# Performance work log

Hardware: AMD Instinct MI355X
Metric: run time of the kernel (lower is better)

The kernel has to match this reference:

```python
import jax, jax.numpy as jnp
import numpy as np

N, E = 20000, 160000
D_NODE_IN, D_EDGE_IN = 256, 64
D = 128          # node/edge feature dim
H = 256          # edge hidden dim
T = 17           # number of keypoint types
EDGE_STEPS, NODE_STEPS = 2, 1


def _w(k, shape):
    return jax.random.normal(k, shape, dtype=jnp.float32) / np.sqrt(shape[-2] if len(shape) > 1 else shape[-1]).astype(np.float32)


def setup_inputs() -> dict:
    key = jax.random.key(0)
    ks = iter(jax.random.split(key, 40))
    inp = {
        'x': jax.random.normal(next(ks), (N, D_NODE_IN), dtype=jnp.float32),
        'edge_attr': jax.random.normal(next(ks), (E, D_EDGE_IN), dtype=jnp.float32),
        'edge_index': jax.random.randint(next(ks), (2, E), 0, N),
        'node_types': jax.random.randint(next(ks), (N,), 0, T),
        # type-routed node embedding: 17 stacked 2-layer MLPs 256->128->128
        'ne_w1': _w(next(ks), (T, D_NODE_IN, D)), 'ne_b1': jnp.zeros((T, D)),
        'ne_w2': _w(next(ks), (T, D, D)),         'ne_b2': jnp.zeros((T, D)),
        # edge embedding 64->128->128
        'ee_w1': _w(next(ks), (D_EDGE_IN, D)), 'ee_b1': jnp.zeros((D,)),
        'ee_w2': _w(next(ks), (D, D)),         'ee_b2': jnp.zeros((D,)),
        # MPLayer edge MLP: [x_i, x_j, e] with skip -> (2*2D + 2D)=768 -> 256 -> 128
        'me_w1': _w(next(ks), (4 * D + 2 * D, H)), 'me_b1': jnp.zeros((H,)),
        'me_w2': _w(next(ks), (H, D)),             'me_b2': jnp.zeros((D,)),
        # MPLayer node update: [x(skip 2D), agg(D)] -> 128
        'mn_w1': _w(next(ks), (2 * D + D, D)), 'mn_b1': jnp.zeros((D,)),
        # classifiers
        'ec_w1': _w(next(ks), (D, D)), 'ec_b1': jnp.zeros((D,)),
        'ec_w2': _w(next(ks), (D, 1)), 'ec_b2': jnp.zeros((1,)),
        'nc_w1': _w(next(ks), (D, D)), 'nc_b1': jnp.zeros((D,)),
        'nc_w2': _w(next(ks), (D, 1)), 'nc_b2': jnp.zeros((1,)),
        'cc_w1': _w(next(ks), (D, D)), 'cc_b1': jnp.zeros((D,)),
        'cc_w2': _w(next(ks), (D, T)), 'cc_b2': jnp.zeros((T,)),
    }
    return inp


def _mlp2(x, w1, b1, w2, b2):
    return jax.nn.relu(x @ w1 + b1) @ w2 + b2


def reference(x, edge_attr, edge_index, node_types,
              ne_w1, ne_b1, ne_w2, ne_b2,
              ee_w1, ee_b1, ee_w2, ee_b2,
              me_w1, me_b1, me_w2, me_b2,
              mn_w1, mn_b1,
              ec_w1, ec_b1, ec_w2, ec_b2,
              nc_w1, nc_b1, nc_w2, nc_b2,
              cc_w1, cc_b1, cc_w2, cc_b2):
    n = x.shape[0]
    # NodeMlpType: run all 17 MLPs, select by node type (same math as masked dispatch)
    h = jax.nn.relu(jnp.einsum('nd,tdk->tnk', x, ne_w1) + ne_b1[:, None, :])   # [T,N,D]
    o = jnp.einsum('tnk,tkm->tnm', h, ne_w2) + ne_b2[:, None, :]               # [T,N,D]
    nf0 = o[node_types, jnp.arange(n)]                                          # [N,D]
    ef0 = _mlp2(edge_attr, ee_w1, ee_b1, ee_w2, ee_b2)                          # [E,D]

    src, dst = edge_index[0], edge_index[1]

    def mp_step(nf, ef):
        nf_c = jnp.concatenate([nf0, nf], axis=1)                               # skip concat [N,2D]
        ef_c = jnp.concatenate([ef0, ef], axis=1)                               # [E,2D]
        m = jnp.concatenate([nf_c[dst], nf_c[src], ef_c], axis=1)               # [E,6D]
        e_new = _mlp2(m, me_w1, me_b1, me_w2, me_b2)                            # [E,D]
        agg = jax.ops.segment_sum(e_new, dst, num_segments=n)                   # aggr='add'
        nf_new = jnp.concatenate([nf_c, agg], axis=1) @ mn_w1 + mn_b1           # [N,D]
        return nf_new, e_new

    nf, ef = nf0, ef0
    for _ in range(EDGE_STEPS):
        nf, ef = mp_step(nf, ef)
    pred_edge = _mlp2(ef, ec_w1, ec_b1, ec_w2, ec_b2).squeeze(-1)               # [E]
    for _ in range(NODE_STEPS):
        nf, ef = mp_step(nf, ef)
    pred_node = _mlp2(nf, nc_w1, nc_b1, nc_w2, nc_b2).squeeze(-1)               # [N]
    pred_class = _mlp2(nf, cc_w1, cc_b1, cc_w2, cc_b2)                          # [N,T]
    return (pred_edge, pred_node, pred_class, nf, ef)
```

## Files before the change

### kernel.cpp

```cpp
#include <hip/hip_runtime.h>
#include <hip/hip_bf16.h>

#define N_NODES 20000
#define N_EDGES 160000
#define DIN_NODE 256
#define DIN_EDGE 64
#define DF 128
#define HH 256
#define TT 17
#define NE_PAD_SLOTS 20544

typedef __attribute__((ext_vector_type(8))) short short8v;
typedef __attribute__((ext_vector_type(4))) float f32x4;

__device__ __forceinline__ unsigned short f2bf(float f) {
  unsigned int u = __builtin_bit_cast(unsigned int, f);
  u += 0x7FFFu + ((u >> 16) & 1u);
  return (unsigned short)(u >> 16);
}

__device__ __forceinline__ float bf2f(unsigned short u) {
  return __builtin_bit_cast(float, (unsigned int)u << 16);
}

__device__ __forceinline__ short8v pack8(float4 a, float4 b) {
  short8v o;
  o[0] = (short)f2bf(a.x); o[1] = (short)f2bf(a.y);
  o[2] = (short)f2bf(a.z); o[3] = (short)f2bf(a.w);
  o[4] = (short)f2bf(b.x); o[5] = (short)f2bf(b.y);
  o[6] = (short)f2bf(b.z); o[7] = (short)f2bf(b.w);
  return o;
}

__global__ __launch_bounds__(256) void k_pack_w(
    const float* __restrict__ w, unsigned short* __restrict__ out,
    int Kdim, int Ndim, int batch) {
  const int tile = blockIdx.x * 4 + (threadIdx.x >> 6);
  const int l = threadIdx.x & 63;
  const int ntTiles = Ndim >> 4;
  const int tilesPer = (Kdim >> 5) * ntTiles;
  if (tile >= tilesPer * batch) return;
  const int bt = tile / tilesPer;
  const int rr = tile - bt * tilesPer;
  const int kt = rr / ntTiles, nt = rr % ntTiles;
  const float* wb = w + (size_t)bt * Kdim * Ndim;
  const int col = (nt << 4) + (l & 15);
  const int k0 = (kt << 5) + ((l >> 4) << 3);
  unsigned short* o = out + (((size_t)tile << 6) + l) * 8;
#pragma unroll
  for (int j = 0; j < 8; ++j) o[j] = f2bf(wb[(size_t)(k0 + j) * Ndim + col]);
}

__global__ void k_count(const int* __restrict__ types, int* __restrict__ cnt) {
  const int n = blockIdx.x * 256 + threadIdx.x;
  if (n < N_NODES) atomicAdd(&cnt[types[n]], 1);
}
__global__ void k_prefix(const int* __restrict__ cnt, int* __restrict__ poff,
                         int* __restrict__ woff) {
  if (threadIdx.x == 0) {
    int cur = 0;
    for (int t = 0; t < TT; ++t) {
      poff[t] = cur; woff[t] = cur;
      cur += (cnt[t] + 31) & ~31;
    }
  }
}
__global__ void k_scatter(const int* __restrict__ types, int* __restrict__ woff,
                          int* __restrict__ bucket) {
  const int n = blockIdx.x * 256 + threadIdx.x;
  if (n < N_NODES) {
    const int pos = atomicAdd(&woff[types[n]], 1);
    bucket[pos] = n;
  }
}

__global__ void k_deg(const int* __restrict__ dstv, int* __restrict__ deg) {
  const int e = blockIdx.x * 256 + threadIdx.x;
  if (e < N_EDGES) atomicAdd(&deg[dstv[e]], 1);
}
__global__ __launch_bounds__(256) void k_scan(const int* __restrict__ deg,
                                              int* __restrict__ rs,
                                              int* __restrict__ wo) {
  __shared__ int partial[256];
  const int t = threadIdx.x;
  const int base = t * 80;
  int s = 0;
  for (int j = 0; j < 80; ++j) {
    const int n = base + j;
    if (n < N_NODES) s += deg[n];
  }
  partial[t] = s;
  __syncthreads();
  for (int off = 1; off < 256; off <<= 1) {
    const int v = (t >= off) ? partial[t - off] : 0;
    __syncthreads();
    partial[t] += v;
    __syncthreads();
  }
  int run = (t > 0) ? partial[t - 1] : 0;
  for (int j = 0; j < 80; ++j) {
    const int n = base + j;
    if (n < N_NODES) {
      rs[n] = run; wo[n] = run;
      run += deg[n];
    }
  }
  if (t == 255) rs[N_NODES] = run;
}
__global__ void k_elist(const int* __restrict__ dstv, int* __restrict__ wo,
                        int* __restrict__ elist, int* __restrict__ ipos) {
  const int e = blockIdx.x * 256 + threadIdx.x;
  if (e < N_EDGES) {
    const int pos = atomicAdd(&wo[dstv[e]], 1);
    elist[pos] = e;
    ipos[e] = pos;
  }
}
__global__ void k_perm_sd(const int* __restrict__ elist,
                          const int* __restrict__ srcv,
                          const int* __restrict__ dstv,
                          int* __restrict__ srcp, int* __restrict__ dstp) {
  const int p = blockIdx.x * 256 + threadIdx.x;
  if (p < N_EDGES) {
    const int e = elist[p];
    srcp[p] = srcv[e];
    dstp[p] = dstv[e];
  }
}

__global__ __launch_bounds__(256) void k_node_embed_mfma(
    const float* __restrict__ x, const int* __restrict__ bucket,
    const int* __restrict__ types,
    const unsigned short* __restrict__ wp1, const float* __restrict__ b1,
    const unsigned short* __restrict__ wp2, const float* __restrict__ b2,
    unsigned short* __restrict__ nf0b) {
  __shared__ __align__(16) unsigned char A[32 * 512];
  __shared__ __align__(16) unsigned char Hb[32 * 256];
  __shared__ int sn[32];
  const int t = threadIdx.x;
  const int r0 = blockIdx.x * 32;
  if (t < 32) sn[t] = bucket[r0 + t];
  __syncthreads();
  if (sn[0] < 0) return;
  const int ty = types[sn[0]];

#pragma unroll
  for (int j = 0; j < 4; ++j) {
    const int q = j * 256 + t;
    const int i = q >> 5, c = q & 31;
    const int nd = sn[i];
    short8v o;
    if (nd >= 0) {
      const float* xr = x + (size_t)nd * DIN_NODE + c * 8;
      o = pack8(*reinterpret_cast<const float4*>(xr),
                *reinterpret_cast<const float4*>(xr + 4));
    } else {
#pragma unroll
      for (int k = 0; k < 8; ++k) o[k] = 0;
    }
    *reinterpret_cast<short8v*>(A + ((i * 512 + c * 16) ^ ((i & 7) << 4))) = o;
  }
  __syncthreads();

  const int w = t >> 6, l = t & 63, lr = l & 15, lg = l >> 4;
  const int sw = (lr & 7) << 4;
  const int row0 = lr, row1 = 16 + lr;

  f32x4 acc[2][2];
#pragma unroll
  for (int mt = 0; mt < 2; ++mt)
#pragma unroll
    for (int q = 0; q < 2; ++q)
#pragma unroll
      for (int r = 0; r < 4; ++r) acc[mt][q][r] = 0.f;

#pragma unroll
  for (int kt = 0; kt < 8; ++kt) {
    const short8v a0 = *reinterpret_cast<const short8v*>(
        A + ((row0 * 512 + kt * 64 + lg * 16) ^ sw));
    const short8v a1 = *reinterpret_cast<const short8v*>(
        A + ((row1 * 512 + kt * 64 + lg * 16) ^ sw));
#pragma unroll
    for (int q = 0; q < 2; ++q) {
      const short8v bq = *reinterpret_cast<const short8v*>(
          wp1 + (((size_t)(ty * 64 + kt * 8 + 2 * w + q) * 64 + l) << 3));
      acc[0][q] = __builtin_amdgcn_mfma_f32_16x16x32_bf16(a0, bq, acc[0][q], 0, 0, 0);
      acc[1][q] = __builtin_amdgcn_mfma_f32_16x16x32_bf16(a1, bq, acc[1][q], 0, 0, 0);
    }
  }
#pragma unroll
  for (int q = 0; q < 2; ++q) {
    const int col = (2 * w + q) * 16 + lr;
    const float bias = b1[ty * DF + col];
#pragma unroll
    for (int mt = 0; mt < 2; ++mt)
#pragma unroll
      for (int r = 0; r < 4; ++r) {
        const int row = mt * 16 + lg * 4 + r;
        *reinterpret_cast<unsigned short*>(
            Hb + ((row * 256 + col * 2) ^ ((row & 7) << 4))) =
            f2bf(fmaxf(acc[mt][q][r] + bias, 0.f));
      }
  }
  __syncthreads();

  f32x4 acc2[2][2];
#pragma unroll
  for (int mt = 0; mt < 2; ++mt)
#pragma unroll
    for (int q = 0; q < 2; ++q)
#pragma unroll
      for (int r = 0; r < 4; ++r) acc2[mt][q][r] = 0.f;
#pragma unroll
  for (int kt = 0; kt < 4; ++kt) {
    const short8v a0 = *reinterpret_cast<const short8v*>(
        Hb + ((row0 * 256 + kt * 64 + lg * 16) ^ sw));
    const short8v a1 = *reinterpret_cast<const short8v*>(
        Hb + ((row1 * 256 + kt * 64 + lg * 16) ^ sw));
#pragma unroll
    for (int q = 0; q < 2; ++q) {
      const short8v bq = *reinterpret_cast<const short8v*>(
          wp2 + (((size_t)(ty * 32 + kt * 8 + 2 * w + q) * 64 + l) << 3));
      acc2[0][q] = __builtin_amdgcn_mfma_f32_16x16x32_bf16(a0, bq, acc2[0][q], 0, 0, 0);
      acc2[1][q] = __builtin_amdgcn_mfma_f32_16x16x32_bf16(a1, bq, acc2[1][q], 0, 0, 0);
    }
  }
#pragma unroll
  for (int q = 0; q < 2; ++q) {
    const int col = (2 * w + q) * 16 + lr;
    const float bias = b2[ty * DF + col];
#pragma unroll
    for (int mt = 0; mt < 2; ++mt)
#pragma unroll
      for (int r = 0; r < 4; ++r) {
        const int row = mt * 16 + lg * 4 + r;
        const int nd = sn[row];
        if (nd >= 0)
          nf0b[(size_t)nd * DF + col] = f2bf(acc2[mt][q][r] + bias);
      }
  }
}

__global__ __launch_bounds__(256) void k_edge_embed_mfma(
    const float* __restrict__ ea, const int* __restrict__ ipos,
    const unsigned short* __restrict__ wp1, const float* __restrict__ b1,
    const unsigned short* __restrict__ wp2, const float* __restrict__ b2,
    unsigned short* __restrict__ ef0p) {
  __shared__ __align__(16) unsigned char A[32 * 128];
  __shared__ __align__(16) unsigned char Hb[32 * 256];
  __shared__ int ip[32];
  const int t = threadIdx.x;
  const int e0 = blockIdx.x * 32;
  if (t < 32) ip[t] = ipos[e0 + t];
  {
    const int i = t >> 3, c = t & 7;
    const float* xr = ea + (size_t)(e0 + i) * DIN_EDGE + c * 8;
    const short8v o = pack8(*reinterpret_cast<const float4*>(xr),
                            *reinterpret_cast<const float4*>(xr + 4));
    *reinterpret_cast<short8v*>(A + ((i * 128 + c * 16) ^ ((i & 7) << 4))) = o;
  }
  __syncthreads();

  const int w = t >> 6, l = t & 63, lr = l & 15, lg = l >> 4;
  const int sw = (lr & 7) << 4;
  const int row0 = lr, row1 = 16 + lr;

  f32x4 acc[2][2];
#pragma unroll
  for (int mt = 0; mt < 2; ++mt)
#pragma unroll
    for (int q = 0; q < 2; ++q)
#pragma unroll
      for (int r = 0; r < 4; ++r) acc[mt][q][r] = 0.f;
#pragma unroll
  for (int kt = 0; kt < 2; ++kt) {
    const short8v a0 = *reinterpret_cast<const short8v*>(
        A + ((row0 * 128 + kt * 64 + lg * 16) ^ sw));
    const short8v a1 = *reinterpret_cast<const short8v*>(
        A + ((row1 * 128 + kt * 64 + lg * 16) ^ sw));
#pragma unroll
    for (int q = 0; q < 2; ++q) {
      const short8v bq = *reinterpret_cast<const short8v*>(
          wp1 + (((size_t)(kt * 8 + 2 * w + q) * 64 + l) << 3));
      acc[0][q] = __builtin_amdgcn_mfma_f32_16x16x32_bf16(a0, bq, acc[0][q], 0, 0, 0);
      acc[1][q] = __builtin_amdgcn_mfma_f32_16x16x32_bf16(a1, bq, acc[1][q], 0, 0, 0);
    }
  }
#pragma unroll
  for (int q = 0; q < 2; ++q) {
    const int col = (2 * w + q) * 16 + lr;
    const float bias = b1[col];
#pragma unroll
    for (int mt = 0; mt < 2; ++mt)
#pragma unroll
      for (int r = 0; r < 4; ++r) {
        const int row = mt * 16 + lg * 4 + r;
        *reinterpret_cast<unsigned short*>(
            Hb + ((row * 256 + col * 2) ^ ((row & 7) << 4))) =
            f2bf(fmaxf(acc[mt][q][r] + bias, 0.f));
      }
  }
  __syncthreads();

  f32x4 acc2[2][2];
#pragma unroll
  for (int mt = 0; mt < 2; ++mt)
#pragma unroll
    for (int q = 0; q < 2; ++q)
#pragma unroll
      for (int r = 0; r < 4; ++r) acc2[mt][q][r] = 0.f;
#pragma unroll
  for (int kt = 0; kt < 4; ++kt) {
    const short8v a0 = *reinterpret_cast<const short8v*>(
        Hb + ((row0 * 256 + kt * 64 + lg * 16) ^ sw));
    const short8v a1 = *reinterpret_cast<const short8v*>(
        Hb + ((row1 * 256 + kt * 64 + lg * 16) ^ sw));
#pragma unroll
    for (int q = 0; q < 2; ++q) {
      const short8v bq = *reinterpret_cast<const short8v*>(
          wp2 + (((size_t)(kt * 8 + 2 * w + q) * 64 + l) << 3));
      acc2[0][q] = __builtin_amdgcn_mfma_f32_16x16x32_bf16(a0, bq, acc2[0][q], 0, 0, 0);
      acc2[1][q] = __builtin_amdgcn_mfma_f32_16x16x32_bf16(a1, bq, acc2[1][q], 0, 0, 0);
    }
  }
#pragma unroll
  for (int q = 0; q < 2; ++q) {
    const int col = (2 * w + q) * 16 + lr;
    const float bias = b2[col];
#pragma unroll
    for (int mt = 0; mt < 2; ++mt)
#pragma unroll
      for (int r = 0; r < 4; ++r) {
        const int row = mt * 16 + lg * 4 + r;
        ef0p[(size_t)ip[row] * DF + col] = f2bf(acc2[mt][q][r] + bias);
      }
  }
}

__global__ __launch_bounds__(256) void k_partial(
    const unsigned short* __restrict__ nf0b, const unsigned short* __restrict__ nfb,
    const unsigned short* __restrict__ wpd, const unsigned short* __restrict__ wps,
    unsigned short* __restrict__ PDo, unsigned short* __restrict__ PSo) {
  __shared__ __align__(16) unsigned char A[32 * 512];
  const int t = threadIdx.x;
  const int n0 = blockIdx.x * 32;
#pragma unroll
  for (int j = 0; j < 4; ++j) {
    const int q = j * 256 + t;
    const int i = q >> 5, c = q & 31;
    const unsigned short* bp = (c < 16)
        ? nf0b + (size_t)(n0 + i) * DF + c * 8
        : nfb + (size_t)(n0 + i) * DF + (c - 16) * 8;
    *reinterpret_cast<short8v*>(A + ((i * 512 + c * 16) ^ ((i & 7) << 4))) =
        *reinterpret_cast<const short8v*>(bp);
  }
  __syncthreads();

  const int w = t >> 6, l = t & 63, lr = l & 15, lg = l >> 4;
  const int swz = (lr & 7) << 4;
  const int r0o = lr * 512 + lg * 16, r1o = (16 + lr) * 512 + lg * 16;

  f32x4 aD[2][4], aS[2][4];
#pragma unroll
  for (int mt = 0; mt < 2; ++mt)
#pragma unroll
    for (int q = 0; q < 4; ++q)
#pragma unroll
      for (int r = 0; r < 4; ++r) { aD[mt][q][r] = 0.f; aS[mt][q][r] = 0.f; }

#pragma unroll
  for (int kt = 0; kt < 8; ++kt) {
    const short8v a0 = *reinterpret_cast<const short8v*>(A + ((r0o + kt * 64) ^ swz));
    const short8v a1 = *reinterpret_cast<const short8v*>(A + ((r1o + kt * 64) ^ swz));
#pragma unroll
    for (int q = 0; q < 4; ++q) {
      const size_t bi = (((size_t)(kt * 16 + 4 * w + q) * 64 + l) << 3);
      const short8v bD = *reinterpret_cast<const short8v*>(wpd + bi);
      const short8v bS = *reinterpret_cast<const short8v*>(wps + bi);
      aD[0][q] = __builtin_amdgcn_mfma_f32_16x16x32_bf16(a0, bD, aD[0][q], 0, 0, 0);
      aD[1][q] = __builtin_amdgcn_mfma_f32_16x16x32_bf16(a1, bD, aD[1][q], 0, 0, 0);
      aS[0][q] = __builtin_amdgcn_mfma_f32_16x16x32_bf16(a0, bS, aS[0][q], 0, 0, 0);
      aS[1][q] = __builtin_amdgcn_mfma_f32_16x16x32_bf16(a1, bS, aS[1][q], 0, 0, 0);
    }
  }
#pragma unroll
  for (int q = 0; q < 4; ++q) {
    const int col = (4 * w + q) * 16 + lr;
#pragma unroll
    for (int mt = 0; mt < 2; ++mt)
#pragma unroll
      for (int r = 0; r < 4; ++r) {
        const int row = mt * 16 + lg * 4 + r;
        PDo[(size_t)(n0 + row) * HH + col] = f2bf(aD[mt][q][r]);
        PSo[(size_t)(n0 + row) * HH + col] = f2bf(aS[mt][q][r]);
      }
  }
}

template <bool OUTF, bool HEAD>
__global__ __launch_bounds__(256) void k_edge_mlp_mfma(
    const unsigned short* __restrict__ ef0, const unsigned short* __restrict__ ef_in,
    unsigned short* __restrict__ ef_out, float* __restrict__ ef_outf,
    const int* __restrict__ srcp, const int* __restrict__ dstp,
    const int* __restrict__ elist,
    const unsigned short* __restrict__ wpe, const float* __restrict__ b1,
    const unsigned short* __restrict__ wp2, const float* __restrict__ b2,
    const unsigned short* __restrict__ PDi, const unsigned short* __restrict__ PSi,
    const unsigned short* __restrict__ wech, const float* __restrict__ hb1,
    const float* __restrict__ hw2, const float* __restrict__ hb2,
    float* __restrict__ out_pe) {
  __shared__ __align__(16) unsigned char A_lds[32 * 512];
  __shared__ __align__(16) unsigned char P_lds[32 * 512];
  __shared__ int sd[2][32];
  __shared__ int se[32];
  __shared__ float hpart[32][8];
  const int t = threadIdx.x;
  const int e0 = blockIdx.x * 32;
  if (t < 32) sd[0][t] = srcp[e0 + t];
  else if (t < 64) sd[1][t - 32] = dstp[e0 + t - 32];
  else if ((OUTF || HEAD) && t < 96) se[t - 64] = elist[e0 + t - 64];

#pragma unroll
  for (int j = 0; j < 4; ++j) {
    const int q = j * 256 + t;
    const int i = q >> 5, c = q & 31;
    const unsigned short* bp = (c < 16)
        ? ef0 + (size_t)(e0 + i) * DF + c * 8
        : ef_in + (size_t)(e0 + i) * DF + (c - 16) * 8;
    *reinterpret_cast<short8v*>(A_lds + ((i * 512 + c * 16) ^ ((i & 7) << 4))) =
        *reinterpret_cast<const short8v*>(bp);
  }
  __syncthreads();

#pragma unroll
  for (int j = 0; j < 4; ++j) {
    const int q = j * 256 + t;
    const int i = q >> 5, c = q & 31;
    const short8v pd = *reinterpret_cast<const short8v*>(
        PDi + (size_t)sd[1][i] * HH + c * 8);
    const short8v ps = *reinterpret_cast<const short8v*>(
        PSi + (size_t)sd[0][i] * HH + c * 8);
    short8v o;
#pragma unroll
    for (int k = 0; k < 8; ++k)
      o[k] = (short)f2bf(bf2f((unsigned short)pd[k]) + bf2f((unsigned short)ps[k]));
    *reinterpret_cast<short8v*>(P_lds + ((i * 512 + c * 16) ^ ((i & 7) << 4))) = o;
  }
  __syncthreads();
// ... 501 lines not shown
  const float* x         = (const float*)d_in[0];
  const float* edge_attr = (const float*)d_in[1];
  const int*   edge_idx  = (const int*)d_in[2];
  const int*   node_ty   = (const int*)d_in[3];
  const float* ne_w1 = (const float*)d_in[4];
  const float* ne_b1 = (const float*)d_in[5];
  const float* ne_w2 = (const float*)d_in[6];
  const float* ne_b2 = (const float*)d_in[7];
  const float* ee_w1 = (const float*)d_in[8];
  const float* ee_b1 = (const float*)d_in[9];
  const float* ee_w2 = (const float*)d_in[10];
  const float* ee_b2 = (const float*)d_in[11];
  const float* me_w1 = (const float*)d_in[12];
  const float* me_b1 = (const float*)d_in[13];
  const float* me_w2 = (const float*)d_in[14];
  const float* me_b2 = (const float*)d_in[15];
  const float* mn_w1 = (const float*)d_in[16];
  const float* mn_b1 = (const float*)d_in[17];
  const float* ec_w1 = (const float*)d_in[18];
  const float* ec_b1 = (const float*)d_in[19];
  const float* ec_w2 = (const float*)d_in[20];
  const float* ec_b2 = (const float*)d_in[21];
  const float* nc_w1 = (const float*)d_in[22];
  const float* nc_b1 = (const float*)d_in[23];
  const float* nc_w2 = (const float*)d_in[24];
  const float* nc_b2 = (const float*)d_in[25];
  const float* cc_w1 = (const float*)d_in[26];
  const float* cc_b1 = (const float*)d_in[27];
  const float* cc_w2 = (const float*)d_in[28];
  const float* cc_b2 = (const float*)d_in[29];

  const int* srcv = edge_idx;
  const int* dstv = edge_idx + N_EDGES;

  unsigned short* nf0b = (unsigned short*)d_ws;
  unsigned short* nf1b = nf0b + (size_t)N_NODES * DF;
  unsigned short* ef0p = nf1b + (size_t)N_NODES * DF;
  unsigned short* ef1p = ef0p + (size_t)N_EDGES * DF;
  unsigned short* wmpD = ef1p + (size_t)N_EDGES * DF;
  unsigned short* wmpS = wmpD + 256 * 256;
  unsigned short* wmeE = wmpS + 256 * 256;
  unsigned short* wme2 = wmeE + 256 * 256;
  unsigned short* wmn  = wme2 + 256 * 128;
  unsigned short* wne1 = wmn + 384 * 128;
  unsigned short* wne2 = wne1 + (size_t)TT * 256 * 128;
  unsigned short* wee1 = wne2 + (size_t)TT * 128 * 128;
  unsigned short* wee2 = wee1 + 64 * 128;
  unsigned short* wec  = wee2 + 128 * 128;
  unsigned short* wnc  = wec + 128 * 128;
  unsigned short* wcc  = wnc + 128 * 128;
  unsigned short* PD   = wcc + 128 * 128;
  unsigned short* PS   = PD + (size_t)N_NODES * HH;
  int* cnt    = (int*)(PS + (size_t)N_NODES * HH);
  int* poff   = cnt + 32;
  int* woff   = poff + 32;
  int* bucket = woff + 32;
  int* deg    = bucket + NE_PAD_SLOTS;
  int* rs     = deg + N_NODES;
  int* wo     = rs + N_NODES + 1;
  int* elist  = wo + N_NODES;
  int* ipos   = elist + N_EDGES;
  int* srcp   = ipos + N_EDGES;
  int* dstp   = srcp + N_EDGES;

  float* out_pe = (float*)d_out;
  float* out_pn = out_pe + N_EDGES;
  float* out_pc = out_pn + N_NODES;
  float* out_nf = out_pc + (size_t)N_NODES * TT;
  float* out_ef = out_nf + (size_t)N_NODES * DF;

  k_pack_w<<<32, 256, 0, stream>>>(me_w1, wmpD, 256, 256, 1);
  k_pack_w<<<32, 256, 0, stream>>>(me_w1 + 256 * 256, wmpS, 256, 256, 1);
  k_pack_w<<<32, 256, 0, stream>>>(me_w1 + 512 * 256, wmeE, 256, 256, 1);
  k_pack_w<<<16, 256, 0, stream>>>(me_w2, wme2, 256, 128, 1);
  k_pack_w<<<24, 256, 0, stream>>>(mn_w1, wmn, 384, 128, 1);
  k_pack_w<<<272, 256, 0, stream>>>(ne_w1, wne1, 256, 128, TT);
  k_pack_w<<<136, 256, 0, stream>>>(ne_w2, wne2, 128, 128, TT);
  k_pack_w<<<4, 256, 0, stream>>>(ee_w1, wee1, 64, 128, 1);
  k_pack_w<<<8, 256, 0, stream>>>(ee_w2, wee2, 128, 128, 1);
  k_pack_w<<<8, 256, 0, stream>>>(ec_w1, wec, 128, 128, 1);
  k_pack_w<<<8, 256, 0, stream>>>(nc_w1, wnc, 128, 128, 1);
  k_pack_w<<<8, 256, 0, stream>>>(cc_w1, wcc, 128, 128, 1);

  hipMemsetAsync(cnt, 0, 32 * sizeof(int), stream);
  hipMemsetAsync(bucket, 0xFF, NE_PAD_SLOTS * sizeof(int), stream);
  k_count<<<(N_NODES + 255) / 256, 256, 0, stream>>>(node_ty, cnt);
  k_prefix<<<1, 64, 0, stream>>>(cnt, poff, woff);
  k_scatter<<<(N_NODES + 255) / 256, 256, 0, stream>>>(node_ty, woff, bucket);

  hipMemsetAsync(deg, 0, N_NODES * sizeof(int), stream);
  k_deg<<<(N_EDGES + 255) / 256, 256, 0, stream>>>(dstv, deg);
  k_scan<<<1, 256, 0, stream>>>(deg, rs, wo);
  k_elist<<<(N_EDGES + 255) / 256, 256, 0, stream>>>(dstv, wo, elist, ipos);
  k_perm_sd<<<(N_EDGES + 255) / 256, 256, 0, stream>>>(elist, srcv, dstv, srcp,
                                                       dstp);

  k_node_embed_mfma<<<NE_PAD_SLOTS / 32, 256, 0, stream>>>(
      x, bucket, node_ty, wne1, ne_b1, wne2, ne_b2, nf0b);
  k_edge_embed_mfma<<<N_EDGES / 32, 256, 0, stream>>>(edge_attr, ipos, wee1,
                                                      ee_b1, wee2, ee_b2, ef0p);

  k_partial<<<N_NODES / 32, 256, 0, stream>>>(nf0b, nf0b, wmpD, wmpS, PD, PS);
  k_edge_mlp_mfma<false, false><<<N_EDGES / 32, 256, 0, stream>>>(
      ef0p, ef0p, ef1p, nullptr, srcp, dstp, elist, wmeE, me_b1, wme2, me_b2,
      PD, PS, nullptr, nullptr, nullptr, nullptr, nullptr);
  k_node_update_mfma<false, true><<<N_NODES / 32, 256, 0, stream>>>(
      nf0b, nf0b, ef1p, rs, (void*)nf1b, wmn, mn_b1, wmpD, wmpS, PD, PS);
  k_edge_mlp_mfma<false, true><<<N_EDGES / 32, 256, 0, stream>>>(
      ef0p, ef1p, ef1p, nullptr, srcp, dstp, elist, wmeE, me_b1, wme2, me_b2,
      PD, PS, wec, ec_b1, ec_w2, ec_b2, out_pe);
  k_node_update_mfma<false, true><<<N_NODES / 32, 256, 0, stream>>>(
      nf0b, nf1b, ef1p, rs, (void*)nf1b, wmn, mn_b1, wmpD, wmpS, PD, PS);
  k_edge_mlp_mfma<true, false><<<N_EDGES / 32, 256, 0, stream>>>(
      ef0p, ef1p, ef1p, out_ef, srcp, dstp, elist, wmeE, me_b1, wme2, me_b2,
      PD, PS, nullptr, nullptr, nullptr, nullptr, nullptr);
  k_node_update_mfma<true, false><<<N_NODES / 32, 256, 0, stream>>>(
      nf0b, nf1b, ef1p, rs, (void*)out_nf, wmn, mn_b1, wmpD, wmpS, PD, PS);

  k_cls_scalar_mfma<false><<<N_NODES / 32, 256, 0, stream>>>(
      (const void*)out_nf, wnc, nc_b1, nc_w2, nc_b2, out_pn);
  k_cls_class_mfma<<<N_NODES / 32, 256, 0, stream>>>(out_nf, wcc, cc_b1, cc_w2,
                                                     cc_b2, out_pc);
}
```

Measured before the change: 628.3 us.

## Fuse weight packing, graph preprocessing, and embedding kernels into fewer launches

```diff
diff --git a/kernel.cpp b/kernel.cpp
--- a/kernel.cpp
+++ b/kernel.cpp
@@ -9,6 +9,7 @@
 #define HH 256
 #define TT 17
 #define NE_PAD_SLOTS 20544
+#define NB_NODE (NE_PAD_SLOTS / 32)
 
 typedef __attribute__((ext_vector_type(8))) short short8v;
 typedef __attribute__((ext_vector_type(4))) float f32x4;
@@ -32,57 +33,61 @@
   return o;
 }
 
-__global__ __launch_bounds__(256) void k_pack_w(
-    const float* __restrict__ w, unsigned short* __restrict__ out,
-    int Kdim, int Ndim, int batch) {
-  const int tile = blockIdx.x * 4 + (threadIdx.x >> 6);
+struct PackPtrs {
+  const float *s0, *s1, *s2, *s3, *s4, *s5, *s6, *s7, *s8, *s9, *s10, *s11;
+  unsigned short *d0, *d1, *d2, *d3, *d4, *d5, *d6, *d7, *d8, *d9, *d10, *d11;
+};
+
+__global__ __launch_bounds__(256) void k_pack_all(PackPtrs P) {
+  const int g = blockIdx.x * 4 + (threadIdx.x >> 6);
   const int l = threadIdx.x & 63;
-  const int ntTiles = Ndim >> 4;
-  const int tilesPer = (Kdim >> 5) * ntTiles;
-  if (tile >= tilesPer * batch) return;
+  if (g >= 2320) return;
+  const float* w; unsigned short* out; int K, N, tile;
+  if (g < 128)       { w = P.s0;  out = P.d0;  K = 256; N = 256; tile = g; }
+  else if (g < 256)  { w = P.s1;  out = P.d1;  K = 256; N = 256; tile = g - 128; }
+  else if (g < 384)  { w = P.s2;  out = P.d2;  K = 256; N = 256; tile = g - 256; }
+  else if (g < 448)  { w = P.s3;  out = P.d3;  K = 256; N = 128; tile = g - 384; }
+  else if (g < 544)  { w = P.s4;  out = P.d4;  K = 384; N = 128; tile = g - 448; }
+  else if (g < 1632) { w = P.s5;  out = P.d5;  K = 256; N = 128; tile = g - 544; }
+  else if (g < 2176) { w = P.s6;  out = P.d6;  K = 128; N = 128; tile = g - 1632; }
+  else if (g < 2192) { w = P.s7;  out = P.d7;  K = 64;  N = 128; tile = g - 2176; }
+  else if (g < 2224) { w = P.s8;  out = P.d8;  K = 128; N = 128; tile = g - 2192; }
+  else if (g < 2256) { w = P.s9;  out = P.d9;  K = 128; N = 128; tile = g - 2224; }
+  else if (g < 2288) { w = P.s10; out = P.d10; K = 128; N = 128; tile = g - 2256; }
+  else               { w = P.s11; out = P.d11; K = 128; N = 128; tile = g - 2288; }
+  const int ntTiles = N >> 4;
+  const int tilesPer = (K >> 5) * ntTiles;
   const int bt = tile / tilesPer;
   const int rr = tile - bt * tilesPer;
-  const int kt = rr / ntTiles, nt = rr % ntTiles;
-  const float* wb = w + (size_t)bt * Kdim * Ndim;
+  const int kt = rr / ntTiles, nt = rr - kt * ntTiles;
+  const float* wb = w + (size_t)bt * K * N;
   const int col = (nt << 4) + (l & 15);
   const int k0 = (kt << 5) + ((l >> 4) << 3);
   unsigned short* o = out + (((size_t)tile << 6) + l) * 8;
 #pragma unroll
-  for (int j = 0; j < 8; ++j) o[j] = f2bf(wb[(size_t)(k0 + j) * Ndim + col]);
-}
-
-__global__ void k_count(const int* __restrict__ types, int* __restrict__ cnt) {
-  const int n = blockIdx.x * 256 + threadIdx.x;
-  if (n < N_NODES) atomicAdd(&cnt[types[n]], 1);
-}
-__global__ void k_prefix(const int* __restrict__ cnt, int* __restrict__ poff,
-                         int* __restrict__ woff) {
-  if (threadIdx.x == 0) {
-    int cur = 0;
-    for (int t = 0; t < TT; ++t) {
-      poff[t] = cur; woff[t] = cur;
-      cur += (cnt[t] + 31) & ~31;
-    }
-  }
-}
-__global__ void k_scatter(const int* __restrict__ types, int* __restrict__ woff,
-                          int* __restrict__ bucket) {
-  const int n = blockIdx.x * 256 + threadIdx.x;
-  if (n < N_NODES) {
-    const int pos = atomicAdd(&woff[types[n]], 1);
-    bucket[pos] = n;
-  }
-}
-
-__global__ void k_deg(const int* __restrict__ dstv, int* __restrict__ deg) {
-  const int e = blockIdx.x * 256 + threadIdx.x;
-  if (e < N_EDGES) atomicAdd(&deg[dstv[e]], 1);
-}
-__global__ __launch_bounds__(256) void k_scan(const int* __restrict__ deg,
-                                              int* __restrict__ rs,
-                                              int* __restrict__ wo) {
+  for (int j = 0; j < 8; ++j) o[j] = f2bf(wb[(size_t)(k0 + j) * N + col]);
+}
+
+__global__ void k_count_deg(const int* __restrict__ types,
+                            const int* __restrict__ dstv,
+                            int* __restrict__ cnt, int* __restrict__ deg) {
+  const int i = blockIdx.x * 256 + threadIdx.x;
+  if (i < N_NODES) atomicAdd(&cnt[types[i]], 1);
+  if (i < N_EDGES) atomicAdd(&deg[dstv[i]], 1);
+}
+
+__global__ __launch_bounds__(256) void k_prefix_scan(
+    const int* __restrict__ cnt, int* __restrict__ woff,
+    const int* __restrict__ deg, int* __restrict__ rs, int* __restrict__ wo) {
   __shared__ int partial[256];
   const int t = threadIdx.x;
+  if (t == 0) {
+    int cur = 0;
+    for (int ty = 0; ty < TT; ++ty) {
+      woff[ty] = cur;
+      cur += (cnt[ty] + 31) & ~31;
+    }
+  }
   const int base = t * 80;
   int s = 0;
   for (int j = 0; j < 80; ++j) {
@@ -107,293 +112,271 @@
   }
   if (t == 255) rs[N_NODES] = run;
 }
-__global__ void k_elist(const int* __restrict__ dstv, int* __restrict__ wo,
-                        int* __restrict__ elist, int* __restrict__ ipos) {
-  const int e = blockIdx.x * 256 + threadIdx.x;
-  if (e < N_EDGES) {
-    const int pos = atomicAdd(&wo[dstv[e]], 1);
-    elist[pos] = e;
-    ipos[e] = pos;
-  }
-}
-__global__ void k_perm_sd(const int* __restrict__ elist,
-                          const int* __restrict__ srcv,
-                          const int* __restrict__ dstv,
-                          int* __restrict__ srcp, int* __restrict__ dstp) {
-  const int p = blockIdx.x * 256 + threadIdx.x;
-  if (p < N_EDGES) {
-    const int e = elist[p];
-    srcp[p] = srcv[e];
-    dstp[p] = dstv[e];
-  }
-}
-
-__global__ __launch_bounds__(256) void k_node_embed_mfma(
+
+__global__ void k_scatter_elist(const int* __restrict__ types,
+                                const int* __restrict__ srcv,
+                                const int* __restrict__ dstv,
+                                int* __restrict__ woff, int* __restrict__ wo,
+                                int* __restrict__ bucket,
+                                int* __restrict__ elist, int* __restrict__ ipos,
+                                int* __restrict__ srcp, int* __restrict__ dstp) {
+  const int i = blockIdx.x * 256 + threadIdx.x;
+  if (i < N_NODES) {
+    const int pos = atomicAdd(&woff[types[i]], 1);
+    bucket[pos] = i;
+  }
+  if (i < N_EDGES) {
+    const int pos = atomicAdd(&wo[dstv[i]], 1);
+    elist[pos] = i;
+    ipos[i] = pos;
+    srcp[pos] = srcv[i];
+    dstp[pos] = dstv[i];
+  }
+}
+
+__global__ __launch_bounds__(256) void k_embed_fused(
     const float* __restrict__ x, const int* __restrict__ bucket,
     const int* __restrict__ types,
     const unsigned short* __restrict__ wp1, const float* __restrict__ b1,
     const unsigned short* __restrict__ wp2, const float* __restrict__ b2,
-    unsigned short* __restrict__ nf0b) {
+    unsigned short* __restrict__ nf0b,
+    const unsigned short* __restrict__ wpd, const unsigned short* __restrict__ wps,
+    unsigned short* __restrict__ PDo, unsigned short* __restrict__ PSo,
+    const float* __restrict__ ea, const int* __restrict__ ipos,
+    const unsigned short* __restrict__ ewp1, const float* __restrict__ eb1,
+    const unsigned short* __restrict__ ewp2, const float* __restrict__ eb2,
+    unsigned short* __restrict__ ef0p) {
   __shared__ __align__(16) unsigned char A[32 * 512];
   __shared__ __align__(16) unsigned char Hb[32 * 256];
-  __shared__ int sn[32];
+  __shared__ int sidx[32];
   const int t = threadIdx.x;
-  const int r0 = blockIdx.x * 32;
-  if (t < 32) sn[t] = bucket[r0 + t];
-  __syncthreads();
-  if (sn[0] < 0) return;
-  const int ty = types[sn[0]];
-
-#pragma unroll
-  for (int j = 0; j < 4; ++j) {
-    const int q = j * 256 + t;
-    const int i = q >> 5, c = q & 31;
-    const int nd = sn[i];
-    short8v o;
-    if (nd >= 0) {
-      const float* xr = x + (size_t)nd * DIN_NODE + c * 8;
-      o = pack8(*reinterpret_cast<const float4*>(xr),
-                *reinterpret_cast<const float4*>(xr + 4));
-    } else {
-#pragma unroll
-      for (int k = 0; k < 8; ++k) o[k] = 0;
-    }
-    *reinterpret_cast<short8v*>(A + ((i * 512 + c * 16) ^ ((i & 7) << 4))) = o;
-  }
-  __syncthreads();
-
   const int w = t >> 6, l = t & 63, lr = l & 15, lg = l >> 4;
   const int sw = (lr & 7) << 4;
   const int row0 = lr, row1 = 16 + lr;
 
-  f32x4 acc[2][2];
-#pragma unroll
-  for (int mt = 0; mt < 2; ++mt)
-#pragma unroll
-    for (int q = 0; q < 2; ++q)
-#pragma unroll
-      for (int r = 0; r < 4; ++r) acc[mt][q][r] = 0.f;
-
-#pragma unroll
-  for (int kt = 0; kt < 8; ++kt) {
-    const short8v a0 = *reinterpret_cast<const short8v*>(
-        A + ((row0 * 512 + kt * 64 + lg * 16) ^ sw));
-    const short8v a1 = *reinterpret_cast<const short8v*>(
-        A + ((row1 * 512 + kt * 64 + lg * 16) ^ sw));
+  if (blockIdx.x < NB_NODE) {
+    const int r0 = blockIdx.x * 32;
+    if (t < 32) sidx[t] = bucket[r0 + t];
+    __syncthreads();
+    if (sidx[0] < 0) return;
+    const int ty = types[sidx[0]];
+
+#pragma unroll
+    for (int j = 0; j < 4; ++j) {
+      const int q = j * 256 + t;
+      const int i = q >> 5, c = q & 31;
+      const int nd = sidx[i];
+      short8v o;
+      if (nd >= 0) {
+        const float* xr = x + (size_t)nd * DIN_NODE + c * 8;
+        o = pack8(*reinterpret_cast<const float4*>(xr),
+                  *reinterpret_cast<const float4*>(xr + 4));
+      } else {
+#pragma unroll
+        for (int k = 0; k < 8; ++k) o[k] = 0;
+      }
+      *reinterpret_cast<short8v*>(A + ((i * 512 + c * 16) ^ ((i & 7) << 4))) = o;
+    }
+    __syncthreads();
+
+    f32x4 acc[2][2];
+#pragma unroll
+    for (int mt = 0; mt < 2; ++mt)
+#pragma unroll
+      for (int q = 0; q < 2; ++q)
+#pragma unroll
+        for (int r = 0; r < 4; ++r) acc[mt][q][r] = 0.f;
+#pragma unroll
+    for (int kt = 0; kt < 8; ++kt) {
+      const short8v a0 = *reinterpret_cast<const short8v*>(
+          A + ((row0 * 512 + kt * 64 + lg * 16) ^ sw));
+      const short8v a1 = *reinterpret_cast<const short8v*>(
+          A + ((row1 * 512 + kt * 64 + lg * 16) ^ sw));
+#pragma unroll
+      for (int q = 0; q < 2; ++q) {
+        const short8v bq = *reinterpret_cast<const short8v*>(
+            wp1 + (((size_t)(ty * 64 + kt * 8 + 2 * w + q) * 64 + l) << 3));
+        acc[0][q] = __builtin_amdgcn_mfma_f32_16x16x32_bf16(a0, bq, acc[0][q], 0, 0, 0);
+        acc[1][q] = __builtin_amdgcn_mfma_f32_16x16x32_bf16(a1, bq, acc[1][q], 0, 0, 0);
+      }
+    }
 #pragma unroll
     for (int q = 0; q < 2; ++q) {
-      const short8v bq = *reinterpret_cast<const short8v*>(
-          wp1 + (((size_t)(ty * 64 + kt * 8 + 2 * w + q) * 64 + l) << 3));
-      acc[0][q] = __builtin_amdgcn_mfma_f32_16x16x32_bf16(a0, bq, acc[0][q], 0, 0, 0);
-      acc[1][q] = __builtin_amdgcn_mfma_f32_16x16x32_bf16(a1, bq, acc[1][q], 0, 0, 0);
-    }
-  }
-#pragma unroll
-  for (int q = 0; q < 2; ++q) {
-    const int col = (2 * w + q) * 16 + lr;
-    const float bias = b1[ty * DF + col];
-#pragma unroll
-    for (int mt = 0; mt < 2; ++mt)
-#pragma unroll
-      for (int r = 0; r < 4; ++r) {
-        const int row = mt * 16 + lg * 4 + r;
-        *reinterpret_cast<unsigned short*>(
-            Hb + ((row * 256 + col * 2) ^ ((row & 7) << 4))) =
-            f2bf(fmaxf(acc[mt][q][r] + bias, 0.f));
-      }
-  }
-  __syncthreads();
-
-  f32x4 acc2[2][2];
-#pragma unroll
-  for (int mt = 0; mt < 2; ++mt)
-#pragma unroll
-    for (int q = 0; q < 2; ++q)
-#pragma unroll
-      for (int r = 0; r < 4; ++r) acc2[mt][q][r] = 0.f;
-#pragma unroll
-  for (int kt = 0; kt < 4; ++kt) {
-    const short8v a0 = *reinterpret_cast<const short8v*>(
-        Hb + ((row0 * 256 + kt * 64 + lg * 16) ^ sw));
-    const short8v a1 = *reinterpret_cast<const short8v*>(
-        Hb + ((row1 * 256 + kt * 64 + lg * 16) ^ sw));
+      const int col = (2 * w + q) * 16 + lr;
+      const float bias = b1[ty * DF + col];
+#pragma unroll
+      for (int mt = 0; mt < 2; ++mt)
+#pragma unroll
+        for (int r = 0; r < 4; ++r) {
+          const int row = mt * 16 + lg * 4 + r;
+          *reinterpret_cast<unsigned short*>(
+              Hb + ((row * 256 + col * 2) ^ ((row & 7) << 4))) =
+              f2bf(fmaxf(acc[mt][q][r] + bias, 0.f));
+        }
+    }
+    __syncthreads();
+
+    f32x4 acc2[2][2];
+#pragma unroll
+    for (int mt = 0; mt < 2; ++mt)
+#pragma unroll
+      for (int q = 0; q < 2; ++q)
+#pragma unroll
+        for (int r = 0; r < 4; ++r) acc2[mt][q][r] = 0.f;
+#pragma unroll
+    for (int kt = 0; kt < 4; ++kt) {
+      const short8v a0 = *reinterpret_cast<const short8v*>(
+          Hb + ((row0 * 256 + kt * 64 + lg * 16) ^ sw));
+      const short8v a1 = *reinterpret_cast<const short8v*>(
+          Hb + ((row1 * 256 + kt * 64 + lg * 16) ^ sw));
+#pragma unroll
+      for (int q = 0; q < 2; ++q) {
+        const short8v bq = *reinterpret_cast<const short8v*>(
+            wp2 + (((size_t)(ty * 32 + kt * 8 + 2 * w + q) * 64 + l) << 3));
+        acc2[0][q] = __builtin_amdgcn_mfma_f32_16x16x32_bf16(a0, bq, acc2[0][q], 0, 0, 0);
+        acc2[1][q] = __builtin_amdgcn_mfma_f32_16x16x32_bf16(a1, bq, acc2[1][q], 0, 0, 0);
+      }
+    }
 #pragma unroll
     for (int q = 0; q < 2; ++q) {
-      const short8v bq = *reinterpret_cast<const short8v*>(
-          wp2 + (((size_t)(ty * 32 + kt * 8 + 2 * w + q) * 64 + l) << 3));
-      acc2[0][q] = __builtin_amdgcn_mfma_f32_16x16x32_bf16(a0, bq, acc2[0][q], 0, 0, 0);
-      acc2[1][q] = __builtin_amdgcn_mfma_f32_16x16x32_bf16(a1, bq, acc2[1][q], 0, 0, 0);
-    }
-  }
-#pragma unroll
-  for (int q = 0; q < 2; ++q) {
-    const int col = (2 * w + q) * 16 + lr;
-    const float bias = b2[ty * DF + col];
-#pragma unroll
-    for (int mt = 0; mt < 2; ++mt)
-#pragma unroll
-      for (int r = 0; r < 4; ++r) {
-        const int row = mt * 16 + lg * 4 + r;
-        const int nd = sn[row];
-        if (nd >= 0)
-          nf0b[(size_t)nd * DF + col] = f2bf(acc2[mt][q][r] + bias);
-      }
-  }
-}
-
-__global__ __launch_bounds__(256) void k_edge_embed_mfma(
-    const float* __restrict__ ea, const int* __restrict__ ipos,
-    const unsigned short* __restrict__ wp1, const float* __restrict__ b1,
-    const unsigned short* __restrict__ wp2, const float* __restrict__ b2,
-    unsigned short* __restrict__ ef0p) {
-  __shared__ __align__(16) unsigned char A[32 * 128];
-  __shared__ __align__(16) unsigned char Hb[32 * 256];
-  __shared__ int ip[32];
-  const int t = threadIdx.x;
-  const int e0 = blockIdx.x * 32;
-  if (t < 32) ip[t] = ipos[e0 + t];
-  {
-    const int i = t >> 3, c = t & 7;
-    const float* xr = ea + (size_t)(e0 + i) * DIN_EDGE + c * 8;
-    const short8v o = pack8(*reinterpret_cast<const float4*>(xr),
-                            *reinterpret_cast<const float4*>(xr + 4));
-    *reinterpret_cast<short8v*>(A + ((i * 128 + c * 16) ^ ((i & 7) << 4))) = o;
-  }
-  __syncthreads();
-
-  const int w = t >> 6, l = t & 63, lr = l & 15, lg = l >> 4;
-  const int sw = (lr & 7) << 4;
-  const int row0 = lr, row1 = 16 + lr;
-
-  f32x4 acc[2][2];
-#pragma unroll
-  for (int mt = 0; mt < 2; ++mt)
-#pragma unroll
-    for (int q = 0; q < 2; ++q)
-#pragma unroll
-      for (int r = 0; r < 4; ++r) acc[mt][q][r] = 0.f;
-#pragma unroll
-  for (int kt = 0; kt < 2; ++kt) {
-    const short8v a0 = *reinterpret_cast<const short8v*>(
-        A + ((row0 * 128 + kt * 64 + lg * 16) ^ sw));
-    const short8v a1 = *reinterpret_cast<const short8v*>(
-        A + ((row1 * 128 + kt * 64 + lg * 16) ^ sw));
+      const int col = (2 * w + q) * 16 + lr;
+      const float bias = b2[ty * DF + col];
+#pragma unroll
+      for (int mt = 0; mt < 2; ++mt)
+#pragma unroll
+        for (int r = 0; r < 4; ++r) {
+          const int row = mt * 16 + lg * 4 + r;
+          const int nd = sidx[row];
+          const unsigned short v = f2bf(acc2[mt][q][r] + bias);
+          if (nd >= 0) nf0b[(size_t)nd * DF + col] = v;
+          *reinterpret_cast<unsigned short*>(
+              A + ((row * 512 + col * 2) ^ ((row & 7) << 4))) = v;
+          *reinterpret_cast<unsigned short*>(
+              A + ((row * 512 + (col + 128) * 2) ^ ((row & 7) << 4))) = v;
+        }
+    }
+    __syncthreads();
+
+    f32x4 aD[2][4], aS[2][4];
+#pragma unroll
+    for (int mt = 0; mt < 2; ++mt)
+#pragma unroll
+      for (int q = 0; q < 4; ++q)
+#pragma unroll
+        for (int r = 0; r < 4; ++r) { aD[mt][q][r] = 0.f; aS[mt][q][r] = 0.f; }
+    const int r0o = lr * 512 + lg * 16, r1o = (16 + lr) * 512 + lg * 16;
+#pragma unroll
+    for (int kt = 0; kt < 8; ++kt) {
+      const short8v a0 = *reinterpret_cast<const short8v*>(A + ((r0o + kt * 64) ^ sw));
+      const short8v a1 = *reinterpret_cast<const short8v*>(A + ((r1o + kt * 64) ^ sw));
+#pragma unroll
+      for (int q = 0; q < 4; ++q) {
+        const size_t bi = (((size_t)(kt * 16 + 4 * w + q) * 64 + l) << 3);
+        const short8v bD = *reinterpret_cast<const short8v*>(wpd + bi);
+        const short8v bS = *reinterpret_cast<const short8v*>(wps + bi);
+        aD[0][q] = __builtin_amdgcn_mfma_f32_16x16x32_bf16(a0, bD, aD[0][q], 0, 0, 0);
+        aD[1][q] = __builtin_amdgcn_mfma_f32_16x16x32_bf16(a1, bD, aD[1][q], 0, 0, 0);
+        aS[0][q] = __builtin_amdgcn_mfma_f32_16x16x32_bf16(a0, bS, aS[0][q], 0, 0, 0);
+        aS[1][q] = __builtin_amdgcn_mfma_f32_16x16x32_bf16(a1, bS, aS[1][q], 0, 0, 0);
+      }
+    }
+#pragma unroll
+    for (int q = 0; q < 4; ++q) {
+      const int col = (4 * w + q) * 16 + lr;
+#pragma unroll
+      for (int mt = 0; mt < 2; ++mt)
+#pragma unroll
+        for (int r = 0; r < 4; ++r) {
+          const int row = mt * 16 + lg * 4 + r;
+          const int nd = sidx[row];
+          if (nd >= 0) {
+            PDo[(size_t)nd * HH + col] = f2bf(aD[mt][q][r]);
+            PSo[(size_t)nd * HH + col] = f2bf(aS[mt][q][r]);
+          }
+        }
+    }
+  } else {
+    const int e0 = (blockIdx.x - NB_NODE) * 32;
+    if (t < 32) sidx[t] = ipos[e0 + t];
+    {
+      const int i = t >> 3, c = t & 7;
+      const float* xr = ea + (size_t)(e0 + i) * DIN_EDGE + c * 8;
+      const short8v o = pack8(*reinterpret_cast<const float4*>(xr),
+                              *reinterpret_cast<const float4*>(xr + 4));
+      *reinterpret_cast<short8v*>(A + ((i * 128 + c * 16) ^ ((i & 7) << 4))) = o;
+    }
+    __syncthreads();
+
+    f32x4 acc[2][2];
+#pragma unroll
+    for (int mt = 0; mt < 2; ++mt)
+#pragma unroll
+      for (int q = 0; q < 2; ++q)
+#pragma unroll
+        for (int r = 0; r < 4; ++r) acc[mt][q][r] = 0.f;
+#pragma unroll
+    for (int kt = 0; kt < 2; ++kt) {
+      const short8v a0 = *reinterpret_cast<const short8v*>(
+          A + ((row0 * 128 + kt * 64 + lg * 16) ^ sw));
+      const short8v a1 = *reinterpret_cast<const short8v*>(
+          A + ((row1 * 128 + kt * 64 + lg * 16) ^ sw));
+#pragma unroll
+      for (int q = 0; q < 2; ++q) {
+        const short8v bq = *reinterpret_cast<const short8v*>(
+            ewp1 + (((size_t)(kt * 8 + 2 * w + q) * 64 + l) << 3));
+        acc[0][q] = __builtin_amdgcn_mfma_f32_16x16x32_bf16(a0, bq, acc[0][q], 0, 0, 0);
+        acc[1][q] = __builtin_amdgcn_mfma_f32_16x16x32_bf16(a1, bq, acc[1][q], 0, 0, 0);
+      }
+    }
 #pragma unroll
     for (int q = 0; q < 2; ++q) {
-      const short8v bq = *reinterpret_cast<const short8v*>(
-          wp1 + (((size_t)(kt * 8 + 2 * w + q) * 64 + l) << 3));
-      acc[0][q] = __builtin_amdgcn_mfma_f32_16x16x32_bf16(a0, bq, acc[0][q], 0, 0, 0);
-      acc[1][q] = __builtin_amdgcn_mfma_f32_16x16x32_bf16(a1, bq, acc[1][q], 0, 0, 0);
-    }
-  }
-#pragma unroll
-  for (int q = 0; q < 2; ++q) {
-    const int col = (2 * w + q) * 16 + lr;
-    const float bias = b1[col];
-#pragma unroll
-    for (int mt = 0; mt < 2; ++mt)
-#pragma unroll
-      for (int r = 0; r < 4; ++r) {
-        const int row = mt * 16 + lg * 4 + r;
-        *reinterpret_cast<unsigned short*>(
-            Hb + ((row * 256 + col * 2) ^ ((row & 7) << 4))) =
-            f2bf(fmaxf(acc[mt][q][r] + bias, 0.f));
-      }
-  }
-  __syncthreads();
-
-  f32x4 acc2[2][2];
-#pragma unroll
-  for (int mt = 0; mt < 2; ++mt)
-#pragma unroll
-    for (int q = 0; q < 2; ++q)
-#pragma unroll
-      for (int r = 0; r < 4; ++r) acc2[mt][q][r] = 0.f;
-#pragma unroll
-  for (int kt = 0; kt < 4; ++kt) {
-    const short8v a0 = *reinterpret_cast<const short8v*>(
-        Hb + ((row0 * 256 + kt * 64 + lg * 16) ^ sw));
-    const short8v a1 = *reinterpret_cast<const short8v*>(
-        Hb + ((row1 * 256 + kt * 64 + lg * 16) ^ sw));
+      const int col = (2 * w + q) * 16 + lr;
+      const float bias = eb1[col];
+#pragma unroll
+      for (int mt = 0; mt < 2; ++mt)
+#pragma unroll
+        for (int r = 0; r < 4; ++r) {
+          const int row = mt * 16 + lg * 4 + r;
+          *reinterpret_cast<unsigned short*>(
+              Hb + ((row * 256 + col * 2) ^ ((row & 7) << 4))) =
+              f2bf(fmaxf(acc[mt][q][r] + bias, 0.f));
+        }
+    }
+    __syncthreads();
+
+    f32x4 acc2[2][2];
+#pragma unroll
+    for (int mt = 0; mt < 2; ++mt)
+#pragma unroll
+      for (int q = 0; q < 2; ++q)
+#pragma unroll
+        for (int r = 0; r < 4; ++r) acc2[mt][q][r] = 0.f;
+#pragma unroll
+    for (int kt = 0; kt < 4; ++kt) {
+      const short8v a0 = *reinterpret_cast<const short8v*>(
+          Hb + ((row0 * 256 + kt * 64 + lg * 16) ^ sw));
+      const short8v a1 = *reinterpret_cast<const short8v*>(
+          Hb + ((row1 * 256 + kt * 64 + lg * 16) ^ sw));
+#pragma unroll
+      for (int q = 0; q < 2; ++q) {
+        const short8v bq = *reinterpret_cast<const short8v*>(
+            ewp2 + (((size_t)(kt * 8 + 2 * w + q) * 64 + l) << 3));
+        acc2[0][q] = __builtin_amdgcn_mfma_f32_16x16x32_bf16(a0, bq, acc2[0][q], 0, 0, 0);
+        acc2[1][q] = __builtin_amdgcn_mfma_f32_16x16x32_bf16(a1, bq, acc2[1][q], 0, 0, 0);
+      }
+    }
 #pragma unroll
     for (int q = 0; q < 2; ++q) {
-      const short8v bq = *reinterpret_cast<const short8v*>(
-          wp2 + (((size_t)(kt * 8 + 2 * w + q) * 64 + l) << 3));
-      acc2[0][q] = __builtin_amdgcn_mfma_f32_16x16x32_bf16(a0, bq, acc2[0][q], 0, 0, 0);
-      acc2[1][q] = __builtin_amdgcn_mfma_f32_16x16x32_bf16(a1, bq, acc2[1][q], 0, 0, 0);
-    }
-  }
-#pragma unroll
-  for (int q = 0; q < 2; ++q) {
-    const int col = (2 * w + q) * 16 + lr;
-    const float bias = b2[col];
-#pragma unroll
-    for (int mt = 0; mt < 2; ++mt)
-#pragma unroll
-      for (int r = 0; r < 4; ++r) {
-        const int row = mt * 16 + lg * 4 + r;
-        ef0p[(size_t)ip[row] * DF + col] = f2bf(acc2[mt][q][r] + bias);
-      }
-  }
-}
-
-__global__ __launch_bounds__(256) void k_partial(
-    const unsigned short* __restrict__ nf0b, const unsigned short* __restrict__ nfb,
-    const unsigned short* __restrict__ wpd, const unsigned short* __restrict__ wps,
-    unsigned short* __restrict__ PDo, unsigned short* __restrict__ PSo) {
-  __shared__ __align__(16) unsigned char A[32 * 512];
-  const int t = threadIdx.x;
-  const int n0 = blockIdx.x * 32;
-#pragma unroll
-  for (int j = 0; j < 4; ++j) {
-    const int q = j * 256 + t;
-    const int i = q >> 5, c = q & 31;
-    const unsigned short* bp = (c < 16)
-        ? nf0b + (size_t)(n0 + i) * DF + c * 8
-        : nfb + (size_t)(n0 + i) * DF + (c - 16) * 8;
-    *reinterpret_cast<short8v*>(A + ((i * 512 + c * 16) ^ ((i & 7) << 4))) =
-        *reinterpret_cast<const short8v*>(bp);
-  }
-  __syncthreads();
-
-  const int w = t >> 6, l = t & 63, lr = l & 15, lg = l >> 4;
-  const int swz = (lr & 7) << 4;
-  const int r0o = lr * 512 + lg * 16, r1o = (16 + lr) * 512 + lg * 16;
-
-  f32x4 aD[2][4], aS[2][4];
-#pragma unroll
-  for (int mt = 0; mt < 2; ++mt)
-#pragma unroll
-    for (int q = 0; q < 4; ++q)
-#pragma unroll
-      for (int r = 0; r < 4; ++r) { aD[mt][q][r] = 0.f; aS[mt][q][r] = 0.f; }
-
-#pragma unroll
-  for (int kt = 0; kt < 8; ++kt) {
-    const short8v a0 = *reinterpret_cast<const short8v*>(A + ((r0o + kt * 64) ^ swz));
-    const short8v a1 = *reinterpret_cast<const short8v*>(A + ((r1o + kt * 64) ^ swz));
-#pragma unroll
-    for (int q = 0; q < 4; ++q) {
-      const size_t bi = (((size_t)(kt * 16 + 4 * w + q) * 64 + l) << 3);
-      const short8v bD = *reinterpret_cast<const short8v*>(wpd + bi);
-      const short8v bS = *reinterpret_cast<const short8v*>(wps + bi);
-      aD[0][q] = __builtin_amdgcn_mfma_f32_16x16x32_bf16(a0, bD, aD[0][q], 0, 0, 0);
-      aD[1][q] = __builtin_amdgcn_mfma_f32_16x16x32_bf16(a1, bD, aD[1][q], 0, 0, 0);
-      aS[0][q] = __builtin_amdgcn_mfma_f32_16x16x32_bf16(a0, bS, aS[0][q], 0, 0, 0);
-      aS[1][q] = __builtin_amdgcn_mfma_f32_16x16x32_bf16(a1, bS, aS[1][q], 0, 0, 0);
-    }
-  }
-#pragma unroll
-  for (int q = 0; q < 4; ++q) {
-    const int col = (4 * w + q) * 16 + lr;
-#pragma unroll
-    for (int mt = 0; mt < 2; ++mt)
-#pragma unroll
-      for (int r = 0; r < 4; ++r) {
-        const int row = mt * 16 + lg * 4 + r;
-        PDo[(size_t)(n0 + row) * HH + col] = f2bf(aD[mt][q][r]);
-        PSo[(size_t)(n0 + row) * HH + col] = f2bf(aS[mt][q][r]);
-      }
+      const int col = (2 * w + q) * 16 + lr;
+      const float bias = eb2[col];
+#pragma unroll
+      for (int mt = 0; mt < 2; ++mt)
+#pragma unroll
+        for (int r = 0; r < 4; ++r) {
+          const int row = mt * 16 + lg * 4 + r;
+          ef0p[(size_t)sidx[row] * DF + col] = f2bf(acc2[mt][q][r] + bias);
+        }
+    }
   }
 }
 
@@ -1001,8 +984,7 @@
   unsigned short* PD   = wcc + 128 * 128;
   unsigned short* PS   = PD + (size_t)N_NODES * HH;
   int* cnt    = (int*)(PS + (size_t)N_NODES * HH);
-  int* poff   = cnt + 32;
-  int* woff   = poff + 32;
+  int* woff   = cnt + 32;
   int* bucket = woff + 32;
   int* deg    = bucket + NE_PAD_SLOTS;
   int* rs     = deg + N_NODES;
@@ -1018,38 +1000,33 @@
   float* out_nf = out_pc + (size_t)N_NODES * TT;
   float* out_ef = out_nf + (size_t)N_NODES * DF;
 
-  k_pack_w<<<32, 256, 0, stream>>>(me_w1, wmpD, 256, 256, 1);
-  k_pack_w<<<32, 256, 0, stream>>>(me_w1 + 256 * 256, wmpS, 256, 256, 1);
-  k_pack_w<<<32, 256, 0, stream>>>(me_w1 + 512 * 256, wmeE, 256, 256, 1);
-  k_pack_w<<<16, 256, 0, stream>>>(me_w2, wme2, 256, 128, 1);
-  k_pack_w<<<24, 256, 0, stream>>>(mn_w1, wmn, 384, 128, 1);
-  k_pack_w<<<272, 256, 0, stream>>>(ne_w1, wne1, 256, 128, TT);
-  k_pack_w<<<136, 256, 0, stream>>>(ne_w2, wne2, 128, 128, TT);
-  k_pack_w<<<4, 256, 0, stream>>>(ee_w1, wee1, 64, 128, 1);
-  k_pack_w<<<8, 256, 0, stream>>>(ee_w2, wee2, 128, 128, 1);
-  k_pack_w<<<8, 256, 0, stream>>>(ec_w1, wec, 128, 128, 1);
-  k_pack_w<<<8, 256, 0, stream>>>(nc_w1, wnc, 128, 128, 1);
-  k_pack_w<<<8, 256, 0, stream>>>(cc_w1, wcc, 128, 128, 1);
+  PackPtrs P;
+  P.s0 = me_w1;            P.d0 = wmpD;
+  P.s1 = me_w1 + 256*256;  P.d1 = wmpS;
+  P.s2 = me_w1 + 512*256;  P.d2 = wmeE;
+  P.s3 = me_w2;            P.d3 = wme2;
+  P.s4 = mn_w1;            P.d4 = wmn;
+  P.s5 = ne_w1;            P.d5 = wne1;
+  P.s6 = ne_w2;            P.d6 = wne2;
+  P.s7 = ee_w1;            P.d7 = wee1;
+  P.s8 = ee_w2;            P.d8 = wee2;
+  P.s9 = ec_w1;            P.d9 = wec;
+  P.s10 = nc_w1;           P.d10 = wnc;
+  P.s11 = cc_w1;           P.d11 = wcc;
+  k_pack_all<<<580, 256, 0, stream>>>(P);
 
   hipMemsetAsync(cnt, 0, 32 * sizeof(int), stream);
+  hipMemsetAsync(deg, 0, N_NODES * sizeof(int), stream);
   hipMemsetAsync(bucket, 0xFF, NE_PAD_SLOTS * sizeof(int), stream);
-  k_count<<<(N_NODES + 255) / 256, 256, 0, stream>>>(node_ty, cnt);
-  k_prefix<<<1, 64, 0, stream>>>(cnt, poff, woff);
-  k_scatter<<<(N_NODES + 255) / 256, 256, 0, stream>>>(node_ty, woff, bucket);
-
-  hipMemsetAsync(deg, 0, N_NODES * sizeof(int), stream);
-  k_deg<<<(N_EDGES + 255) / 256, 256, 0, stream>>>(dstv, deg);
-  k_scan<<<1, 256, 0, stream>>>(deg, rs, wo);
-  k_elist<<<(N_EDGES + 255) / 256, 256, 0, stream>>>(dstv, wo, elist, ipos);
-  k_perm_sd<<<(N_EDGES + 255) / 256, 256, 0, stream>>>(elist, srcv, dstv, srcp,
-                                                       dstp);
-
-  k_node_embed_mfma<<<NE_PAD_SLOTS / 32, 256, 0, stream>>>(
-      x, bucket, node_ty, wne1, ne_b1, wne2, ne_b2, nf0b);
-  k_edge_embed_mfma<<<N_EDGES / 32, 256, 0, stream>>>(edge_attr, ipos, wee1,
-                                                      ee_b1, wee2, ee_b2, ef0p);
-
-  k_partial<<<N_NODES / 32, 256, 0, stream>>>(nf0b, nf0b, wmpD, wmpS, PD, PS);
+  k_count_deg<<<(N_EDGES + 255) / 256, 256, 0, stream>>>(node_ty, dstv, cnt, deg);
+  k_prefix_scan<<<1, 256, 0, stream>>>(cnt, woff, deg, rs, wo);
+  k_scatter_elist<<<(N_EDGES + 255) / 256, 256, 0, stream>>>(
+      node_ty, srcv, dstv, woff, wo, bucket, elist, ipos, srcp, dstp);
+
+  k_embed_fused<<<NB_NODE + N_EDGES / 32, 256, 0, stream>>>(
+      x, bucket, node_ty, wne1, ne_b1, wne2, ne_b2, nf0b, wmpD, wmpS, PD, PS,
+      edge_attr, ipos, wee1, ee_b1, wee2, ee_b2, ef0p);
+
   k_edge_mlp_mfma<false, false><<<N_EDGES / 32, 256, 0, stream>>>(
       ef0p, ef0p, ef1p, nullptr, srcp, dstp, elist, wmeE, me_b1, wme2, me_b2,
       PD, PS, nullptr, nullptr, nullptr, nullptr, nullptr);
```

After: 575.3 us. 8.4% less time.
